# Kernel optimization log

Measured on AMD Instinct MI355X. Metric: run time of the kernel, lower is better.

Reference implementation:

```python
import jax, jax.numpy as jnp
import numpy as np

_EPS = 1e-12  # Keras l2_normalize epsilon guard


def _l2norm(v, axis):
    return v / jnp.maximum(jnp.linalg.norm(v, axis=axis, keepdims=True), _EPS)


def setup_inputs() -> dict:
    key = jax.random.key(0)
    k1, k2 = jax.random.split(key)
    x = jax.random.normal(k1, (8, 512, 512), dtype=jnp.float32)   # (batch, seq, d)
    E = jax.random.normal(k2, (50257, 512), dtype=jnp.float32)    # (vocab, d) embedding table
    return {"x": x, "E": E}


def reference(x, E):
    # Original: embeddings L2-normalized along axis=1, transposed to (d, vocab);
    # x L2-normalized along axis=2; per-batch-step dot + argmax over vocab.
    xn = _l2norm(x, axis=2)          # (b, s, d)
    En = _l2norm(E, axis=1)          # (v, d)
    s = jnp.einsum('bsd,vd->bsv', xn, En)  # cosine scores, one fused batched GEMM
    return jnp.argmax(s, axis=2)     # (b, s) nearest-embedding indices
```

## Files before the change

kernel.cpp:

```cpp
#include <hip/hip_runtime.h>
#include <hip/hip_bf16.h>
#include <hip/hip_fp16.h>
#include <stdint.h>

#define DDIM  512
#define NROWS 4096
#define VOCAB 50257
#define BM2 256
#define BN 128
#define BK 64
#define BK3 32
#define NT ((VOCAB + BN - 1) / BN)
#define NT2 ((NT + 1) / 2)
#define NTP (NT2 * 2)
#define VC2 16
#define RB2 (NROWS / BM2)
#define EB_ROWS (NTP * BN)
#define TW16 (NTP * 32)
#define TAU16 0.04f
#define TAU1  0.02f
#define LISTCAP (1 << 18)

typedef short bf16x8 __attribute__((ext_vector_type(8)));
typedef float f32x4  __attribute__((ext_vector_type(4)));

__device__ __forceinline__ unsigned int enc_f32(float f) {
    unsigned int u = __float_as_uint(f);
    return (u & 0x80000000u) ? ~u : (u | 0x80000000u);
}
__device__ __forceinline__ float dec_f32(unsigned int e) {
    unsigned int u = (e & 0x80000000u) ? (e & 0x7fffffffu) : ~e;
    return __uint_as_float(u);
}
__device__ __forceinline__ unsigned short bf16_rne(float f) {
    unsigned int u = __float_as_uint(f);
    u += 0x7fffu + ((u >> 16) & 1u);
    return (unsigned short)(u >> 16);
}
__device__ __forceinline__ void gload16(const short* g, short* l) {
    __builtin_amdgcn_global_load_lds(
        (const __attribute__((address_space(1))) void*)g,
        (__attribute__((address_space(3))) void*)l, 16, 0, 0);
}
__device__ __forceinline__ uint4 pack8(float4 a, float4 b) {
    uint4 wv;
    wv.x = ((unsigned)bf16_rne(a.y) << 16) | bf16_rne(a.x);
    wv.y = ((unsigned)bf16_rne(a.w) << 16) | bf16_rne(a.z);
    wv.z = ((unsigned)bf16_rne(b.y) << 16) | bf16_rne(b.x);
    wv.w = ((unsigned)bf16_rne(b.w) << 16) | bf16_rne(b.z);
    return wv;
}


__global__ void k_conv_x(const float* __restrict__ X, short* __restrict__ Xb,
                         unsigned* __restrict__ cnt) {
    int i = blockIdx.x * 256 + threadIdx.x;
    if (i == 0) *cnt = 0u;
    const float4* p = (const float4*)X + (size_t)i * 2;
    float4 a = p[0], b = p[1];
    *(uint4*)(Xb + (size_t)i * 8) = pack8(a, b);
}

__global__ void k_conv_e(const float* __restrict__ E, short* __restrict__ Eb,
                         float* __restrict__ invn) {
    int lane = threadIdx.x & 63;
    int wid  = blockIdx.x * 4 + (threadIdx.x >> 6);
    int nw   = gridDim.x * 4;
    for (int r = wid; r < EB_ROWS; r += nw) {
        if (r < VOCAB) {
            const float4* p = (const float4*)(E + (size_t)r * DDIM) + lane * 2;
            float4 a = p[0], b = p[1];
            float s = a.x*a.x + a.y*a.y + a.z*a.z + a.w*a.w
                    + b.x*b.x + b.y*b.y + b.z*b.z + b.w*b.w;
            #pragma unroll
            for (int off = 32; off; off >>= 1) s += __shfl_xor(s, off, 64);
            *(uint4*)(Eb + (size_t)r * DDIM + lane * 8) = pack8(a, b);
            if (lane == 0) invn[r] = 1.0f / fmaxf(sqrtf(s), 1e-12f);
        } else {
            uint4 z; z.x = z.y = z.z = z.w = 0u;
            *(uint4*)(Eb + (size_t)r * DDIM + lane * 8) = z;
            if (lane == 0) invn[r] = 0.0f;
        }
    }
}


__device__ __forceinline__ void stA(const short* Xb, short* Ab,
                                    int row0, int k0, int tid) {
    #pragma unroll
    for (int i = 0; i < 2; ++i) {
        int c = tid + i * 512;
        int r = c >> 2, g = c & 3;
        int gs = (g ^ ((r >> 1) & 3)) * 8;
        gload16(Xb + (size_t)(row0 + r) * DDIM + k0 + gs, Ab + c * 8);
    }
}
__device__ __forceinline__ void stB(const short* Eb, short* Bb,
                                    int v0, int k0, int tid) {
    int r = tid >> 2, g = tid & 3;
    int gs = (g ^ ((r >> 1) & 3)) * 8;
    gload16(Eb + (size_t)(v0 + r) * DDIM + k0 + gs, Bb + tid * 8);
}

__global__ __launch_bounds__(512)
void k_gemm_fast16(const short* __restrict__ Xb, const short* __restrict__ Eb,
                   const float* __restrict__ invn, unsigned short* __restrict__ tm)
{
    extern __shared__ __align__(16) short smem[];
    short* As = smem;
    short* Bs = smem + 3 * BM2 * BK3;

    const int tid  = threadIdx.x;
    const int lane = tid & 63;
    const int w    = tid >> 6;
    const int wm   = w >> 1;
    const int wn   = w & 1;
    const int row0 = blockIdx.x * BM2;
    const int l15  = lane & 15, lhi = lane >> 4;

    for (int p = blockIdx.y; p < NT2; p += VC2) {
        const int t0 = 2 * p;
        const int v0 = t0 * BN, v1 = v0 + BN;
        f32x4 acc[2][4][4];
        #pragma unroll
        for (int j = 0; j < 2; ++j)
            #pragma unroll
            for (int m = 0; m < 4; ++m)
                #pragma unroll
                for (int n = 0; n < 4; ++n)
                    acc[j][m][n] = 0.0f;

        stA(Xb, As, row0, 0, tid);
        stB(Eb, Bs, v0, 0, tid);
        stB(Eb, Bs + BN * BK3, v1, 0, tid);
        stA(Xb, As + BM2 * BK3, row0, BK3, tid);
        stB(Eb, Bs + 2 * BN * BK3, v0, BK3, tid);
        stB(Eb, Bs + 3 * BN * BK3, v1, BK3, tid);
        asm volatile("s_waitcnt vmcnt(4)" ::: "memory");
        __builtin_amdgcn_s_barrier();
        __builtin_amdgcn_sched_barrier(0);

        #pragma unroll
        for (int kt = 0; kt < DDIM / BK3; ++kt) {
            const short* Ac = As + (kt % 3) * (BM2 * BK3);
            const short* B0 = Bs + (kt % 3) * (2 * BN * BK3);
            const short* B1 = B0 + BN * BK3;
            if (kt + 2 < DDIM / BK3) {
                short* An = As + ((kt + 2) % 3) * (BM2 * BK3);
                short* Bn = Bs + ((kt + 2) % 3) * (2 * BN * BK3);
                stA(Xb, An, row0, (kt + 2) * BK3, tid);
                stB(Eb, Bn, v0, (kt + 2) * BK3, tid);
                stB(Eb, Bn + BN * BK3, v1, (kt + 2) * BK3, tid);
            }

            __builtin_amdgcn_s_setprio(1);
            bf16x8 av[4], bv0[4], bv1[4];
            #pragma unroll
            for (int m = 0; m < 4; ++m) {
                int r  = wm * 64 + m * 16 + l15;
                int ke = (lhi ^ ((r >> 1) & 3)) << 3;
                av[m] = *(const bf16x8*)(Ac + r * BK3 + ke);
            }
            #pragma unroll
            for (int n = 0; n < 4; ++n) {
                int c  = wn * 64 + n * 16 + l15;
                int ke = (lhi ^ ((c >> 1) & 3)) << 3;
                bv0[n] = *(const bf16x8*)(B0 + c * BK3 + ke);
                bv1[n] = *(const bf16x8*)(B1 + c * BK3 + ke);
            }
            #pragma unroll
            for (int m = 0; m < 4; ++m)
                #pragma unroll
                for (int n = 0; n < 4; ++n) {
                    acc[0][m][n] = __builtin_amdgcn_mfma_f32_16x16x32_bf16(
                        av[m], bv0[n], acc[0][m][n], 0, 0, 0);
                    acc[1][m][n] = __builtin_amdgcn_mfma_f32_16x16x32_bf16(
                        av[m], bv1[n], acc[1][m][n], 0, 0, 0);
                }
            __builtin_amdgcn_s_setprio(0);

            if (kt < DDIM / BK3 - 1) {
                if (kt + 2 < DDIM / BK3)
                    asm volatile("s_waitcnt vmcnt(4)" ::: "memory");
                else
                    asm volatile("s_waitcnt vmcnt(0)" ::: "memory");
                __builtin_amdgcn_s_barrier();
                __builtin_amdgcn_sched_barrier(0);
            }
        }

        #pragma unroll
        for (int j = 0; j < 2; ++j) {
            const int vj = v0 + j * BN;
            float inv[4];
            #pragma unroll
            for (int n = 0; n < 4; ++n) inv[n] = invn[vj + wn * 64 + n * 16 + l15];
            const int slotbase = (t0 + j) * 32 + wn * 16 + l15;
            #pragma unroll
            for (int m = 0; m < 4; ++m) {
                #pragma unroll
                for (int q = 0; q < 4; ++q) {
                    float s = fmaxf(
                        fmaxf(acc[j][m][0][q] * inv[0], acc[j][m][1][q] * inv[1]),
                        fmaxf(acc[j][m][2][q] * inv[2], acc[j][m][3][q] * inv[3]));
                    int row = row0 + wm * 64 + m * 16 + lhi * 4 + q;
                    tm[(size_t)row * TW16 + slotbase] = __half_as_ushort(__float2half(s));
                }
            }
        }

        asm volatile("s_waitcnt vmcnt(0)" ::: "memory");
        __builtin_amdgcn_s_barrier();
        __builtin_amdgcn_sched_barrier(0);
    }
}

__global__ void k_select16(const unsigned short* __restrict__ tm,
                           unsigned* __restrict__ list, unsigned* __restrict__ cnt,
                           unsigned long long* __restrict__ keys) {
    int row  = blockIdx.x * 4 + (threadIdx.x >> 6);
    int lane = threadIdx.x & 63;
    if (lane == 0) keys[row] = 0ull;
    const unsigned short* p = tm + (size_t)row * TW16;
    float m = -INFINITY;
    for (int c = lane; c < TW16 / 8; c += 64) {
        bf16x8 v = *(const bf16x8*)(p + c * 8);
        #pragma unroll
        for (int k = 0; k < 8; ++k)
            m = fmaxf(m, __half2float(__ushort_as_half((unsigned short)v[k])));
    }
    #pragma unroll
    for (int off = 32; off; off >>= 1) m = fmaxf(m, __shfl_xor(m, off, 64));
    float th = m - TAU16;
    for (int c = lane; c < TW16 / 8; c += 64) {
        bf16x8 v = *(const bf16x8*)(p + c * 8);
        #pragma unroll
        for (int k = 0; k < 8; ++k) {
            if (__half2float(__ushort_as_half((unsigned short)v[k])) >= th) {
                unsigned slot = atomicAdd(cnt, 1u);
                if (slot < LISTCAP)
                    list[slot] = ((unsigned)row << 14) | (unsigned)(c * 8 + k);
            }
        }
    }
}

__global__ __launch_bounds__(256)
void k_rescore4(const float* __restrict__ X, const float* __restrict__ E,
                const float* __restrict__ invn,
                const unsigned* __restrict__ list, const unsigned* __restrict__ cnt,
                unsigned long long* __restrict__ keys) {
    unsigned n = *cnt; if (n > LISTCAP) n = LISTCAP;
    int lane = (int)threadIdx.x & 63;
    int nn   = lane >> 4;
    int part = lane & 15;
    unsigned wv = blockIdx.x * 4 + ((unsigned)threadIdx.x >> 6);
    unsigned nw = gridDim.x * 4;
    for (unsigned ci = wv; ci < n; ci += nw) {
        unsigned e = list[ci];
        int row  = (int)(e >> 14);
        int slot = (int)(e & 16383u);
        int col  = (slot >> 5) * 128 + ((slot >> 4) & 1) * 64 + nn * 16 + (slot & 15);
        if (col < VOCAB) {
            const float4* xp = (const float4*)(X + (size_t)row * DDIM + part * 32);
            const float4* ep = (const float4*)(E + (size_t)col * DDIM + part * 32);
            double s = 0.0;
            #pragma unroll
            for (int d = 0; d < 8; ++d) {
                float4 a = xp[d], b = ep[d];
                s = fma((double)a.x, (double)b.x, s);
                s = fma((double)a.y, (double)b.y, s);
                s = fma((double)a.z, (double)b.z, s);
                s = fma((double)a.w, (double)b.w, s);
            }
            s += __shfl_xor(s, 1, 64);
            s += __shfl_xor(s, 2, 64);
            s += __shfl_xor(s, 4, 64);
            s += __shfl_xor(s, 8, 64);
            if (part == 0) {
                float fs = (float)(s * (double)invn[col]);
                unsigned long long key = ((unsigned long long)enc_f32(fs) << 32)
                                       | (unsigned long long)(0xffffffffu - (unsigned)col);
                atomicMax(keys + row, key);
            }
        }
    }
}

__global__ void k_final(const unsigned long long* __restrict__ keys,
                        int* __restrict__ out) {
    int i = blockIdx.x * 256 + threadIdx.x;
    if (i < NROWS)
        out[i] = (int)(0xffffffffu - (unsigned int)(keys[i] & 0xffffffffull));
}


__global__ __launch_bounds__(512)
void k_gemm_fast1(const short* __restrict__ Xb, const short* __restrict__ Eb,
                  const float* __restrict__ invn, float* __restrict__ tm)
{
    constexpr int TW = NT * 2;
    __shared__ __align__(16) short Ab[BM2 * BK];
    __shared__ __align__(16) short Bb[BN  * BK];

    const int tid  = threadIdx.x;
    const int lane = tid & 63;
    const int w    = tid >> 6;
    const int wm   = w >> 1;
    const int wn   = w & 1;
    const int row0 = blockIdx.x * BM2;
    const int l15  = lane & 15, lhi = lane >> 4;

    for (int t = blockIdx.y; t < NT; t += VC2) {
        const int v0 = t * BN;
        f32x4 acc[4][4];
        #pragma unroll
        for (int m = 0; m < 4; ++m)
            #pragma unroll
            for (int n = 0; n < 4; ++n)
                acc[m][n] = 0.0f;

        for (int kt = 0; kt < DDIM / BK; ++kt) {
            const int k0 = kt * BK;
            #pragma unroll
            for (int i = 0; i < 4; ++i) {
                int c = tid + i * 512;
                int r = c >> 3, g = c & 7;
                int gs = (g ^ (r & 7)) * 8;
                gload16(Xb + (size_t)(row0 + r) * DDIM + k0 + gs, Ab + c * 8);
            }
            #pragma unroll
            for (int i = 0; i < 2; ++i) {
                int c = tid + i * 512;
                int r = c >> 3, g = c & 7;
                int gs = (g ^ (r & 7)) * 8;
                gload16(Eb + (size_t)(v0 + r) * DDIM + k0 + gs, Bb + c * 8);
            }
            __syncthreads();
            #pragma unroll
            for (int ks = 0; ks < 2; ++ks) {
                bf16x8 av[4], bv[4];
                #pragma unroll
                for (int m = 0; m < 4; ++m) {
                    int r  = wm * 64 + m * 16 + l15;
                    int ke = (ks * 32 + lhi * 8) ^ ((r & 7) << 3);
                    av[m] = *(const bf16x8*)(Ab + r * BK + ke);
                }
                #pragma unroll
                for (int n = 0; n < 4; ++n) {
                    int c  = wn * 64 + n * 16 + l15;
                    int ke = (ks * 32 + lhi * 8) ^ ((c & 7) << 3);
                    bv[n] = *(const bf16x8*)(Bb + c * BK + ke);
                }
                #pragma unroll
                for (int m = 0; m < 4; ++m)
                    #pragma unroll
                    for (int n = 0; n < 4; ++n)
                        acc[m][n] = __builtin_amdgcn_mfma_f32_16x16x32_bf16(
                            av[m], bv[n], acc[m][n], 0, 0, 0);
            }
            __syncthreads();
        }

        float inv[4];
        #pragma unroll
        for (int n = 0; n < 4; ++n) inv[n] = invn[v0 + wn * 64 + n * 16 + l15];
        #pragma unroll
        for (int m = 0; m < 4; ++m) {
            #pragma unroll
            for (int j = 0; j < 4; ++j) {
                float v = fmaxf(fmaxf(acc[m][0][j] * inv[0], acc[m][1][j] * inv[1]),
                                fmaxf(acc[m][2][j] * inv[2], acc[m][3][j] * inv[3]));
                #pragma unroll
                for (int off = 1; off < 16; off <<= 1)
                    v = fmaxf(v, __shfl_xor(v, off, 64));
                if (l15 == 0) {
                    int row = row0 + wm * 64 + m * 16 + lhi * 4 + j;
                    tm[(size_t)row * TW + t * 2 + wn] = v;
                }
            }
        }
    }
}

__global__ void k_select1(const float* __restrict__ tm,
                          unsigned* __restrict__ list, unsigned* __restrict__ cnt,
                          unsigned long long* __restrict__ keys) {
    constexpr int TW = NT * 2;
    int row  = blockIdx.x * 4 + (threadIdx.x >> 6);
    int lane = threadIdx.x & 63;
    if (lane == 0) keys[row] = 0ull;
    const float* p = tm + (size_t)row * TW;
    float m = -INFINITY;
    for (int i = lane; i < TW; i += 64) m = fmaxf(m, p[i]);
    #pragma unroll
    for (int off = 32; off; off >>= 1) m = fmaxf(m, __shfl_xor(m, off, 64));
    float th = m - TAU1;
    for (int i = lane; i < TW; i += 64) {
        if (p[i] >= th) {
            unsigned slot = atomicAdd(cnt, 1u);
            if (slot < LISTCAP) list[slot] = ((unsigned)row << 14) | (unsigned)i;
        }
    }
}

__global__ __launch_bounds__(256)
void k_rescore64(const float* __restrict__ X, const float* __restrict__ E,
                 const float* __restrict__ invn,
                 const unsigned* __restrict__ list, const unsigned* __restrict__ cnt,
                 unsigned long long* __restrict__ keys) {
    unsigned n = *cnt; if (n > LISTCAP) n = LISTCAP;
    for (unsigned ci = blockIdx.x; ci < n; ci += gridDim.x) {
        unsigned e = list[ci];
        int row = (int)(e >> 14);
        int idx = (int)(e & 16383u);
        int v0  = (idx >> 1) * BN + (idx & 1) * 64;
        int col  = v0 + ((int)threadIdx.x >> 2);
        int part = (int)threadIdx.x & 3;
        if (col < VOCAB) {
            const float4* xp = (const float4*)(X + (size_t)row * DDIM + part * 128);
            const float4* ep = (const float4*)(E + (size_t)col * DDIM + part * 128);
            double s = 0.0;
            #pragma unroll 8
            for (int d = 0; d < 32; ++d) {
                float4 a = xp[d], b = ep[d];
                s = fma((double)a.x, (double)b.x, s);
                s = fma((double)a.y, (double)b.y, s);
                s = fma((double)a.z, (double)b.z, s);
                s = fma((double)a.w, (double)b.w, s);
            }
            s += __shfl_xor(s, 1, 64);
            s += __shfl_xor(s, 2, 64);
            if (part == 0) {
                float fs = (float)(s * (double)invn[col]);
                unsigned long long key = ((unsigned long long)enc_f32(fs) << 32)
                                       | (unsigned long long)(0xffffffffu - (unsigned)col);
                atomicMax(keys + row, key);
            }
        }
    }
}


#define BM 128
#define VC 33

__global__ void k_init_fb(unsigned int* rowmax, unsigned long long* keys) {
    int i = blockIdx.x * 256 + threadIdx.x;
    if (i < NROWS) { rowmax[i] = 0u; keys[i] = 0ull; }
}

__global__ void k_enorm(const float* __restrict__ E, float* __restrict__ invn) {
    int lane = threadIdx.x & 63;
    int wid  = blockIdx.x * 4 + (threadIdx.x >> 6);
    int nw   = gridDim.x * 4;
    for (int r = wid; r < VOCAB; r += nw) {
        const float4* p = (const float4*)(E + (size_t)r * DDIM);
        float4 a = p[lane];
        float4 b = p[lane + 64];
        float s = a.x*a.x + a.y*a.y + a.z*a.z + a.w*a.w
                + b.x*b.x + b.y*b.y + b.z*b.z + b.w*b.w;
        #pragma unroll
        for (int off = 32; off; off >>= 1) s += __shfl_xor(s, off, 64);
        if (lane == 0) invn[r] = 1.0f / fmaxf(sqrtf(s), 1e-12f);
    }
}

__device__ __noinline__ void rescore1(const float* __restrict__ X,
                                      const float* __restrict__ E,
                                      float iv, int row, int col,
                                      unsigned long long* keys) {
    const float4* xp = (const float4*)(X + (size_t)row * DDIM);
    const float4* ep = (const float4*)(E + (size_t)col * DDIM);
    double a0 = 0.0, a1 = 0.0, a2 = 0.0, a3 = 0.0;
    for (int d = 0; d < DDIM / 4; ++d) {
        float4 x4 = xp[d], e4 = ep[d];
        a0 = fma((double)x4.x, (double)e4.x, a0);
        a1 = fma((double)x4.y, (double)e4.y, a1);
        a2 = fma((double)x4.z, (double)e4.z, a2);
        a3 = fma((double)x4.w, (double)e4.w, a3);
    }
    float fs = (float)((((a0 + a1) + (a2 + a3))) * (double)iv);
    unsigned long long key = ((unsigned long long)enc_f32(fs) << 32)
                           | (unsigned long long)(0xffffffffu - (unsigned int)col);
    atomicMax(keys + row, key);
}

template <int PASS>
__global__ __launch_bounds__(256, 2)
void k_gemm_fb(const float* __restrict__ X, const float* __restrict__ E,
               const float* __restrict__ invn,
               unsigned int* __restrict__ rowmax,
               unsigned long long* __restrict__ keys)
{
    __shared__ __align__(16) short Abuf[BM * BK];
    __shared__ __align__(16) short Bbuf[BN * BK];

    const int tid  = threadIdx.x;
    const int lane = tid & 63;
    const int w    = tid >> 6;
    const int wm   = w >> 1, wn = w & 1;
    const int row0 = blockIdx.y * BM;
    const int l15  = lane & 15, lhi = lane >> 4;

    float rmax[4][4];
    float thr[4][4];
    #pragma unroll
    for (int m = 0; m < 4; ++m)
        #pragma unroll
        for (int j = 0; j < 4; ++j) {
            rmax[m][j] = -INFINITY;
            if (PASS == 2) {
                int row = row0 + wm * 64 + m * 16 + lhi * 4 + j;
                thr[m][j] = dec_f32(rowmax[row]) - TAU1;
            }
        }

    for (int t = blockIdx.x; t < NT; t += VC) {
        const int v0 = t * BN;
        f32x4 acc[4][4];
        #pragma unroll
        for (int m = 0; m < 4; ++m)
            #pragma unroll
            for (int n = 0; n < 4; ++n)
                acc[m][n] = 0.0f;

        for (int kt = 0; kt < DDIM / BK; ++kt) {
            const int k0 = kt * BK;
            #pragma unroll
            for (int i = 0; i < 4; ++i) {
                int f  = tid + i * 256;
                int r  = f >> 3;
                int ks = (f & 7) * 8;
                const float* src = X + (size_t)(row0 + r) * DDIM + k0 + ks;
                float4 aa = *(const float4*)src;
                float4 bb = *(const float4*)(src + 4);
                *(uint4*)(Abuf + r * BK + (ks ^ ((r & 7) << 3))) = pack8(aa, bb);
            }
            #pragma unroll
            for (int i = 0; i < 4; ++i) {
                int f  = tid + i * 256;
                int r  = f >> 3;
                int ks = (f & 7) * 8;
                float4 aa = {0.f,0.f,0.f,0.f}, bb = {0.f,0.f,0.f,0.f};
                if (v0 + r < VOCAB) {
                    const float* src = E + (size_t)(v0 + r) * DDIM + k0 + ks;
                    aa = *(const float4*)src;
                    bb = *(const float4*)(src + 4);
                }
                *(uint4*)(Bbuf + r * BK + (ks ^ ((r & 7) << 3))) = pack8(aa, bb);
            }
            __syncthreads();
            #pragma unroll
            for (int ks = 0; ks < 2; ++ks) {
                bf16x8 av[4], bv[4];
                #pragma unroll
                for (int m = 0; m < 4; ++m) {
                    int r  = wm * 64 + m * 16 + l15;
                    int ke = (ks * 32 + lhi * 8) ^ ((r & 7) << 3);
                    av[m] = *(const bf16x8*)(Abuf + r * BK + ke);
                }
                #pragma unroll
                for (int n = 0; n < 4; ++n) {
                    int c  = wn * 64 + n * 16 + l15;
                    int ke = (ks * 32 + lhi * 8) ^ ((c & 7) << 3);
                    bv[n] = *(const bf16x8*)(Bbuf + c * BK + ke);
                }
                #pragma unroll
                for (int m = 0; m < 4; ++m)
                    #pragma unroll
                    for (int n = 0; n < 4; ++n)
                        acc[m][n] = __builtin_amdgcn_mfma_f32_16x16x32_bf16(
                            av[m], bv[n], acc[m][n], 0, 0, 0);
            }
            __syncthreads();
        }

        float inv[4]; int colv[4];
        #pragma unroll
        for (int n = 0; n < 4; ++n) {
            int c = v0 + wn * 64 + n * 16 + l15;
            colv[n] = c;
            inv[n] = (c < VOCAB) ? invn[c] : 0.0f;
        }
        if (PASS == 1) {
            #pragma unroll
            for (int m = 0; m < 4; ++m)
                #pragma unroll
                for (int n = 0; n < 4; ++n)
                    if (colv[n] < VOCAB) {
                        #pragma unroll
                        for (int j = 0; j < 4; ++j)
                            rmax[m][j] = fmaxf(rmax[m][j], acc[m][n][j] * inv[n]);
                    }
        } else {
            #pragma unroll
            for (int m = 0; m < 4; ++m)
                #pragma unroll
                for (int n = 0; n < 4; ++n)
                    if (colv[n] < VOCAB) {
                        #pragma unroll
                        for (int j = 0; j < 4; ++j) {
                            float sc = acc[m][n][j] * inv[n];
                            if (sc >= thr[m][j]) {
                                int row = row0 + wm * 64 + m * 16 + lhi * 4 + j;
                                rescore1(X, E, inv[n], row, colv[n], keys);
                            }
                        }
                    }
        }
    }

    if (PASS == 1) {
        #pragma unroll
        for (int m = 0; m < 4; ++m)
            #pragma unroll
            for (int j = 0; j < 4; ++j) {
                float v = rmax[m][j];
                #pragma unroll
                for (int off = 1; off < 16; off <<= 1)
                    v = fmaxf(v, __shfl_xor(v, off, 64));
                if (l15 == 0) {
                    int row = row0 + wm * 64 + m * 16 + lhi * 4 + j;
                    atomicMax(rowmax + row, enc_f32(v));
                }
            }
    }
}


extern "C" void kernel_launch(void* const* d_in, const int* in_sizes, int n_in,
                              void* d_out, int out_size, void* d_ws, size_t ws_size,
                              hipStream_t stream) {
    const float* X = (const float*)d_in[0];
    const float* E = (const float*)d_in[1];
    int* out = (int*)d_out;
    char* ws = (char*)d_ws;

    const size_t sz_Eb    = (size_t)EB_ROWS * DDIM * 2;
    const size_t sz_Xb    = (size_t)NROWS * DDIM * 2;
    const size_t sz_invn  = (size_t)EB_ROWS * 4;
    const size_t sz_keys  = (size_t)NROWS * 8;
    const size_t sz_list  = (size_t)LISTCAP * 4;
    const size_t fixed    = sz_Eb + sz_Xb + sz_invn + sz_keys + sz_list + 256;
    const size_t sz_tm16  = (size_t)NROWS * TW16 * 2;
    const size_t sz_tm1   = (size_t)NROWS * (NT * 2) * 4;

    int tier = 0;
    if (ws_size >= fixed + sz_tm16)     tier = 16;
    else if (ws_size >= fixed + sz_tm1) tier = 1;

    if (tier) {
        const size_t sz_tm = (tier == 16) ? sz_tm16 : sz_tm1;
        short* Eb   = (short*)(ws);
        short* Xb   = (short*)(ws + sz_Eb);
        float* invn = (float*)(ws + sz_Eb + sz_Xb);
        char*  tmb  = ws + sz_Eb + sz_Xb + sz_invn;
        unsigned long long* keys = (unsigned long long*)(tmb + sz_tm);
        unsigned* list = (unsigned*)((char*)keys + sz_keys);
        unsigned* cnt  = (unsigned*)((char*)list + sz_list);

        k_conv_x<<<(NROWS * DDIM / 8) / 256, 256, 0, stream>>>(X, Xb, cnt);
        k_conv_e<<<2048, 256, 0, stream>>>(E, Eb, invn);
        dim3 g(RB2, VC2);
        if (tier == 16) {
            const size_t smem = (size_t)3 * (BM2 * BK3 + 2 * BN * BK3) * sizeof(short);
            k_gemm_fast16<<<g, 512, smem, stream>>>(Xb, Eb, invn, (unsigned short*)tmb);
            k_select16<<<NROWS / 4, 256, 0, stream>>>((unsigned short*)tmb, list, cnt, keys);
            k_rescore4<<<2048, 256, 0, stream>>>(X, E, invn, list, cnt, keys);
        } else {
            k_gemm_fast1<<<g, 512, 0, stream>>>(Xb, Eb, invn, (float*)tmb);
            k_select1<<<NROWS / 4, 256, 0, stream>>>((float*)tmb, list, cnt, keys);
            k_rescore64<<<2048, 256, 0, stream>>>(X, E, invn, list, cnt, keys);
        }
        k_final<<<(NROWS + 255) / 256, 256, 0, stream>>>(keys, out);
    } else {
        float* invn = (float*)ws;
        size_t off0 = ((size_t)VOCAB * 4 + 255) & ~(size_t)255;
        unsigned int* rowmax = (unsigned int*)(ws + off0);
        size_t off1 = off0 + (((size_t)NROWS * 4 + 255) & ~(size_t)255);
        unsigned long long* keys = (unsigned long long*)(ws + off1);

        k_init_fb<<<(NROWS + 255) / 256, 256, 0, stream>>>(rowmax, keys);
        k_enorm<<<1024, 256, 0, stream>>>(E, invn);
        dim3 g(VC, NROWS / BM);
        k_gemm_fb<1><<<g, 256, 0, stream>>>(X, E, invn, rowmax, keys);
        k_gemm_fb<2><<<g, 256, 0, stream>>>(X, E, invn, rowmax, keys);
        k_final<<<(NROWS + 255) / 256, 256, 0, stream>>>(keys, out);
    }
}
```

Before: 379.6 us.

## Switch GEMM to double-buffered BK=64 tiles with 8-way XOR swizzle

```diff
diff --git a/kernel.cpp b/kernel.cpp
--- a/kernel.cpp
+++ b/kernel.cpp
@@ -9,7 +9,6 @@
 #define BM2 256
 #define BN 128
 #define BK 64
-#define BK3 32
 #define NT ((VOCAB + BN - 1) / BN)
 #define NT2 ((NT + 1) / 2)
 #define NTP (NT2 * 2)
@@ -88,18 +87,22 @@
 __device__ __forceinline__ void stA(const short* Xb, short* Ab,
                                     int row0, int k0, int tid) {
     #pragma unroll
+    for (int i = 0; i < 4; ++i) {
+        int c = tid + i * 512;
+        int r = c >> 3, g = c & 7;
+        int gs = (g ^ (r & 7)) * 8;
+        gload16(Xb + (size_t)(row0 + r) * DDIM + k0 + gs, Ab + c * 8);
+    }
+}
+__device__ __forceinline__ void stB(const short* Eb, short* Bb,
+                                    int v0, int k0, int tid) {
+    #pragma unroll
     for (int i = 0; i < 2; ++i) {
         int c = tid + i * 512;
-        int r = c >> 2, g = c & 3;
-        int gs = (g ^ ((r >> 1) & 3)) * 8;
-        gload16(Xb + (size_t)(row0 + r) * DDIM + k0 + gs, Ab + c * 8);
-    }
-}
-__device__ __forceinline__ void stB(const short* Eb, short* Bb,
-                                    int v0, int k0, int tid) {
-    int r = tid >> 2, g = tid & 3;
-    int gs = (g ^ ((r >> 1) & 3)) * 8;
-    gload16(Eb + (size_t)(v0 + r) * DDIM + k0 + gs, Bb + tid * 8);
+        int r = c >> 3, g = c & 7;
+        int gs = (g ^ (r & 7)) * 8;
+        gload16(Eb + (size_t)(v0 + r) * DDIM + k0 + gs, Bb + c * 8);
+    }
 }
 
 __global__ __launch_bounds__(512)
@@ -108,7 +111,7 @@
 {
     extern __shared__ __align__(16) short smem[];
     short* As = smem;
-    short* Bs = smem + 3 * BM2 * BK3;
+    short* Bs = smem + 2 * BM2 * BK;
 
     const int tid  = threadIdx.x;
     const int lane = tid & 63;
@@ -132,61 +135,52 @@
 
         stA(Xb, As, row0, 0, tid);
         stB(Eb, Bs, v0, 0, tid);
-        stB(Eb, Bs + BN * BK3, v1, 0, tid);
-        stA(Xb, As + BM2 * BK3, row0, BK3, tid);
-        stB(Eb, Bs + 2 * BN * BK3, v0, BK3, tid);
-        stB(Eb, Bs + 3 * BN * BK3, v1, BK3, tid);
-        asm volatile("s_waitcnt vmcnt(4)" ::: "memory");
-        __builtin_amdgcn_s_barrier();
-        __builtin_amdgcn_sched_barrier(0);
-
-        #pragma unroll
-        for (int kt = 0; kt < DDIM / BK3; ++kt) {
-            const short* Ac = As + (kt % 3) * (BM2 * BK3);
-            const short* B0 = Bs + (kt % 3) * (2 * BN * BK3);
-            const short* B1 = B0 + BN * BK3;
-            if (kt + 2 < DDIM / BK3) {
-                short* An = As + ((kt + 2) % 3) * (BM2 * BK3);
-                short* Bn = Bs + ((kt + 2) % 3) * (2 * BN * BK3);
-                stA(Xb, An, row0, (kt + 2) * BK3, tid);
-                stB(Eb, Bn, v0, (kt + 2) * BK3, tid);
-                stB(Eb, Bn + BN * BK3, v1, (kt + 2) * BK3, tid);
-            }
-
+        stB(Eb, Bs + BN * BK, v1, 0, tid);
+        __syncthreads();
+
+        #pragma unroll
+        for (int kt = 0; kt < DDIM / BK; ++kt) {
+            const int cur = kt & 1;
+            if (kt + 1 < DDIM / BK) {
+                short* An = As + (cur ^ 1) * (BM2 * BK);
+                short* Bn = Bs + (cur ^ 1) * (2 * BN * BK);
+                stA(Xb, An, row0, (kt + 1) * BK, tid);
+                stB(Eb, Bn, v0, (kt + 1) * BK, tid);
+                stB(Eb, Bn + BN * BK, v1, (kt + 1) * BK, tid);
+            }
+
+            const short* Ac = As + cur * (BM2 * BK);
+            const short* B0 = Bs + cur * (2 * BN * BK);
+            const short* B1 = B0 + BN * BK;
             __builtin_amdgcn_s_setprio(1);
-            bf16x8 av[4], bv0[4], bv1[4];
-            #pragma unroll
-            for (int m = 0; m < 4; ++m) {
-                int r  = wm * 64 + m * 16 + l15;
-                int ke = (lhi ^ ((r >> 1) & 3)) << 3;
-                av[m] = *(const bf16x8*)(Ac + r * BK3 + ke);
-            }
-            #pragma unroll
-            for (int n = 0; n < 4; ++n) {
-                int c  = wn * 64 + n * 16 + l15;
-                int ke = (lhi ^ ((c >> 1) & 3)) << 3;
-                bv0[n] = *(const bf16x8*)(B0 + c * BK3 + ke);
-                bv1[n] = *(const bf16x8*)(B1 + c * BK3 + ke);
-            }
-            #pragma unroll
-            for (int m = 0; m < 4; ++m)
+            #pragma unroll
+            for (int ks = 0; ks < 2; ++ks) {
+                bf16x8 av[4], bv0[4], bv1[4];
+                #pragma unroll
+                for (int m = 0; m < 4; ++m) {
+                    int r  = wm * 64 + m * 16 + l15;
+                    int ke = (ks * 32 + lhi * 8) ^ ((r & 7) << 3);
+                    av[m] = *(const bf16x8*)(Ac + r * BK + ke);
+                }
                 #pragma unroll
                 for (int n = 0; n < 4; ++n) {
-                    acc[0][m][n] = __builtin_amdgcn_mfma_f32_16x16x32_bf16(
-                        av[m], bv0[n], acc[0][m][n], 0, 0, 0);
-                    acc[1][m][n] = __builtin_amdgcn_mfma_f32_16x16x32_bf16(
-                        av[m], bv1[n], acc[1][m][n], 0, 0, 0);
-                }
+                    int c  = wn * 64 + n * 16 + l15;
+                    int ke = (ks * 32 + lhi * 8) ^ ((c & 7) << 3);
+                    bv0[n] = *(const bf16x8*)(B0 + c * BK + ke);
+                    bv1[n] = *(const bf16x8*)(B1 + c * BK + ke);
+                }
+                #pragma unroll
+                for (int m = 0; m < 4; ++m)
+                    #pragma unroll
+                    for (int n = 0; n < 4; ++n) {
+                        acc[0][m][n] = __builtin_amdgcn_mfma_f32_16x16x32_bf16(
+                            av[m], bv0[n], acc[0][m][n], 0, 0, 0);
+                        acc[1][m][n] = __builtin_amdgcn_mfma_f32_16x16x32_bf16(
+                            av[m], bv1[n], acc[1][m][n], 0, 0, 0);
+                    }
+            }
             __builtin_amdgcn_s_setprio(0);
-
-            if (kt < DDIM / BK3 - 1) {
-                if (kt + 2 < DDIM / BK3)
-                    asm volatile("s_waitcnt vmcnt(4)" ::: "memory");
-                else
-                    asm volatile("s_waitcnt vmcnt(0)" ::: "memory");
-                __builtin_amdgcn_s_barrier();
-                __builtin_amdgcn_sched_barrier(0);
-            }
+            __syncthreads();
         }
 
         #pragma unroll
@@ -208,10 +202,6 @@
                 }
             }
         }
-
-        asm volatile("s_waitcnt vmcnt(0)" ::: "memory");
-        __builtin_amdgcn_s_barrier();
-        __builtin_amdgcn_sched_barrier(0);
     }
 }
 
@@ -664,7 +654,7 @@
         k_conv_e<<<2048, 256, 0, stream>>>(E, Eb, invn);
         dim3 g(RB2, VC2);
         if (tier == 16) {
-            const size_t smem = (size_t)3 * (BM2 * BK3 + 2 * BN * BK3) * sizeof(short);
+            const size_t smem = (size_t)2 * (BM2 * BK + 2 * BN * BK) * sizeof(short);
             k_gemm_fast16<<<g, 512, smem, stream>>>(Xb, Eb, invn, (unsigned short*)tmb);
             k_select16<<<NROWS / 4, 256, 0, stream>>>((unsigned short*)tmb, list, cnt, keys);
             k_rescore4<<<2048, 256, 0, stream>>>(X, E, invn, list, cnt, keys);
```

Result: slower. 456.6 us (+20.3%).
